# Optimization experiments

Hardware: AMD Instinct MI355X
Metric: run time of the kernel (lower is better)

Reference implementation:

```python
import jax, jax.numpy as jnp
import numpy as np

EPS = 1e-6


def _rmsnorm(x, w, eps=EPS):
    # x: (..., d); normalize over last dim
    ms = jnp.mean(jnp.square(x), axis=-1, keepdims=True)
    return x * jax.lax.rsqrt(ms + eps) * w


def setup_inputs() -> dict:
    key = jax.random.key(0)
    ks = jax.random.split(key, 5)
    B, S, D = 2, 2048, 2048
    n_heads, n_kv = 16, 4
    d_head = D // n_heads  # 128
    sd = 1.0 / np.sqrt(D)
    return {
        "x": jax.random.normal(ks[0], (B, S, D), dtype=jnp.float32),
        "wq": jax.random.normal(ks[1], (D, n_heads * d_head), dtype=jnp.float32) * sd,
        "wk": jax.random.normal(ks[2], (D, n_kv * d_head), dtype=jnp.float32) * sd,
        "wv": jax.random.normal(ks[3], (D, n_kv * d_head), dtype=jnp.float32) * sd,
        "wo": jax.random.normal(ks[4], (D, D), dtype=jnp.float32) * sd,
        "q_norm_w": jnp.ones((d_head,), dtype=jnp.float32),
        "k_norm_w": jnp.ones((d_head,), dtype=jnp.float32),
    }


def reference(x, wq, wk, wv, wo, q_norm_w, k_norm_w):
    B, S, D = x.shape
    n_heads, n_kv = 16, 4
    groups = n_heads // n_kv
    d_head = D // n_heads

    # QKV projections (bias=False)
    q = (x @ wq).reshape(B, S, n_kv, groups, d_head)  # q heads grouped by kv head
    k = (x @ wk).reshape(B, S, n_kv, d_head)
    v = (x @ wv).reshape(B, S, n_kv, d_head)

    # qk RMSNorm over d_head
    q = _rmsnorm(q, q_norm_w)
    k = _rmsnorm(k, k_norm_w)

    # GQA attention without materializing expanded K/V:
    # scores: (B, n_kv, groups, S_q, S_k)
    scale = 1.0 / jnp.sqrt(jnp.asarray(d_head, dtype=x.dtype))
    scores = jnp.einsum('bskgd,btkd->bkgst', q, k) * scale
    causal = jnp.tril(jnp.ones((S, S), dtype=bool))
    scores = jnp.where(causal, scores, jnp.asarray(-jnp.inf, dtype=scores.dtype))
    attn = jax.nn.softmax(scores, axis=-1)
    out = jnp.einsum('bkgst,btkd->bskgd', attn, v)  # (B, S, n_kv, groups, d_head)
    out = out.reshape(B, S, D)
    return out @ wo
```

## Files before the change

kernel.cpp:

```cpp
#include <hip/hip_runtime.h>
#include <hip/hip_bf16.h>
#include <stdint.h>

typedef unsigned short u16;
typedef __attribute__((ext_vector_type(8))) short short8;
typedef __attribute__((ext_vector_type(4))) float f32x4;
typedef __attribute__((ext_vector_type(16))) float f32x16;

__device__ __forceinline__ u16 f2bf(float f){
  union { __hip_bfloat16 h; u16 u; } v; v.h = __float2bfloat16(f); return v.u;
}
__device__ __forceinline__ float bf2f(u16 h){
  union { uint32_t u; float f; } v; v.u = ((uint32_t)h) << 16;
  return v.f;
}
__device__ __forceinline__ f32x4 mfma16(short8 a, short8 b, f32x4 c){
  return __builtin_amdgcn_mfma_f32_16x16x32_bf16(a, b, c, 0, 0, 0);
}
__device__ __forceinline__ f32x16 mfma32(short8 a, short8 b, f32x16 c){
  return __builtin_amdgcn_mfma_f32_32x32x16_bf16(a, b, c, 0, 0, 0);
}
__device__ __forceinline__ void gl_lds16(const u16* g, u16* l){
  __builtin_amdgcn_global_load_lds((const __attribute__((address_space(1))) void*)g,
                                   (__attribute__((address_space(3))) void*)l, 16, 0, 0);
}
template<int N> __device__ __forceinline__ void waitvm(){
  if constexpr (N==0) asm volatile("s_waitcnt vmcnt(0)" ::: "memory");
  else if constexpr (N==2) asm volatile("s_waitcnt vmcnt(2)" ::: "memory");
  else if constexpr (N==4) asm volatile("s_waitcnt vmcnt(4)" ::: "memory");
  else if constexpr (N==8) asm volatile("s_waitcnt vmcnt(8)" ::: "memory");
  else static_assert(N==0 || N==2 || N==4 || N==8, "unsupported vmcnt");
}
__device__ __forceinline__ void phase_sep(){
  __builtin_amdgcn_sched_barrier(0);
  __builtin_amdgcn_s_barrier();
  __builtin_amdgcn_sched_barrier(0);
}
__device__ __forceinline__ uint32_t cvtpk(float lo, float hi){
  uint32_t r;
  asm("v_cvt_pk_bf16_f32 %0, %1, %2" : "=v"(r) : "v"(lo), "v"(hi));
  return r;
}

__global__ __launch_bounds__(256) void prep(const float* __restrict__ x,
    const float* __restrict__ wq, const float* __restrict__ wk,
    const float* __restrict__ wv, const float* __restrict__ wo,
    u16* __restrict__ xbf, u16* __restrict__ wqkvT, u16* __restrict__ woT)
{
  __shared__ float tile[32][33];
  int bid = blockIdx.x;
  const int tid = threadIdx.x;
  if (bid < 8192){
    const int i = bid*256 + tid;
    const float4 v = ((const float4*)x)[i];
    ushort4 pk;
    pk.x = f2bf(v.x); pk.y = f2bf(v.y); pk.z = f2bf(v.z); pk.w = f2bf(v.w);
    ((ushort4*)xbf)[i] = pk;
    return;
  }
  bid -= 8192;
  const float* src; u16* dst; int C, bx, by;
  if (bid < 4096){ src = wq; dst = wqkvT; C = 2048; bx = bid & 63; by = bid >> 6; }
  else if (bid < 8192){ bid -= 4096; src = wo; dst = woT; C = 2048; bx = bid & 63; by = bid >> 6; }
  else if (bid < 9216){ bid -= 8192; src = wk; dst = wqkvT + 2048*2048; C = 512; bx = bid & 15; by = bid >> 4; }
  else { bid -= 9216; src = wv; dst = wqkvT + 2560*2048; C = 512; bx = bid & 15; by = bid >> 4; }
  const int R = 2048;
  const int tx = tid & 31, ty = tid >> 5;
  const int c0 = bx << 5, r0 = by << 5;
  #pragma unroll
  for (int i=0;i<4;i++)
    tile[ty + (i<<3)][tx] = src[(size_t)(r0 + ty + (i<<3))*C + c0 + tx];
  __syncthreads();
  #pragma unroll
  for (int i=0;i<4;i++)
    dst[(size_t)(c0 + ty + (i<<3))*R + r0 + tx] = f2bf(tile[tx][ty + (i<<3)]);
}

__global__ __launch_bounds__(256) void norm_vt(u16* __restrict__ qkv,
    const float* __restrict__ kw, u16* __restrict__ vT)
{
  const int tid = threadIdx.x;
  int bid = blockIdx.x;
  if (bid < 4096){
    const int lane = tid & 63;
    const int rid = bid*4 + (tid >> 6);
    const int row = rid >> 2;
    const int slot = rid & 3;
    u16* p = qkv + (size_t)row*3072 + 2048 + slot*128 + (lane<<1);
    const u16 r0 = p[0], r1 = p[1];
    const float a = bf2f(r0), c = bf2f(r1);
    float ss = a*a + c*c;
    #pragma unroll
    for (int off=1; off<64; off<<=1) ss += __shfl_xor(ss, off);
    const float sc = rsqrtf(ss*(1.0f/128.0f) + 1e-6f);
    const float w0 = kw[lane<<1], w1 = kw[(lane<<1)+1];
    p[0] = f2bf(a*sc*w0);
    p[1] = f2bf(c*sc*w1);
    return;
  }
  bid -= 4096;
  __shared__ u16 tile[32][33];
  const int tx = tid & 31, ty = tid >> 5;
  const int s0 = (bid & 63) << 5;
  const int d0 = ((bid >> 6) & 3) << 5;
  const int bk = bid >> 8; const int b = bk >> 2, kv = bk & 3;
  const u16* src = qkv + (size_t)b*2048*3072 + 2560 + kv*128;
  #pragma unroll
  for (int i=0;i<4;i++)
    tile[ty + (i<<3)][tx] = src[(size_t)(s0 + ty + (i<<3))*3072 + d0 + tx];
  __syncthreads();
  u16* dst = vT + (size_t)((b<<2)+kv)*128*2048;
  #pragma unroll
  for (int i=0;i<4;i++)
    dst[(size_t)(d0 + ty + (i<<3))*2048 + s0 + tx] = tile[tx][ty + (i<<3)];
}

__global__ __launch_bounds__(512, 2) void gemm192(const u16* __restrict__ A,
    const u16* __restrict__ BT, u16* __restrict__ Cp,
    int M, int N, int K, int ldc)
{
  constexpr int ASZ  = 128*64;
  constexpr int BSZ  = 64*64;
  constexpr int DBUF = 2*ASZ + 3*BSZ;
  __shared__ u16 lds[2*DBUF];
  const int tid = threadIdx.x;
  const int w = tid >> 6, lane = tid & 63;
  const int l15 = lane & 15, lg = lane >> 4;
  const int wm = w >> 2, wn = w & 3;
  const int nbx = N / 192;
  const int nwg = gridDim.x;
  int bid = blockIdx.x;
  bid = (bid & 7) * (nwg >> 3) + (bid >> 3);
  const int m0 = (bid / nbx) << 8;
  const int n0 = (bid % nbx) * 192;

  const u16* gA0 = A  + (size_t)m0*K;
  const u16* gA1 = gA0 + (size_t)128*K;
  const u16* gB  = BT + (size_t)n0*K;

  auto slotA = [&](int d, int h)->u16*{ return lds + d*DBUF + h*ASZ; };
  auto slotB = [&](int d, int s)->u16*{ return lds + d*DBUF + 2*ASZ + s*BSZ; };

  auto stage128 = [&](const u16* gbase, int kt, u16* sbase){
    #pragma unroll
    for (int i=0;i<2;i++){
      const int p = (i<<9) + tid;
      const int row = p>>3, sg = (p&7) ^ (row&7);
      gl_lds16(gbase + (size_t)row*K + (kt<<6) + (sg<<3), sbase + (p<<3));
    }
  };
  auto stage64 = [&](const u16* gbase, int kt, u16* sbase){
    const int row = tid>>3, sg = (tid&7) ^ (row&7);
    gl_lds16(gbase + (size_t)row*K + (kt<<6) + (sg<<3), sbase + (tid<<3));
  };
  auto stA = [&](int kt, int d){ stage128(gA0, kt, slotA(d,0));
                                 stage128(gA1, kt, slotA(d,1)); };
  auto stB = [&](int kt, int d){ stage64(gB,               kt, slotB(d,0));
                                 stage64(gB + (size_t) 64*K, kt, slotB(d,1));
                                 stage64(gB + (size_t)128*K, kt, slotB(d,2)); };
  auto frag_at = [&](const u16* buf, int lrow, int kk)->short8{
    const int s = ((kk<<2)+lg) ^ (lrow&7);
    return *(const short8*)(buf + (((lrow<<3)+s)<<3));
  };

  short8 af[4][2], bfe[2][2], bfo[2];
  f32x4 acc[8][3];
  #pragma unroll
  for (int m=0;m<8;m++)
    #pragma unroll
    for (int n=0;n<3;n++) acc[m][n] = (f32x4){0.f,0.f,0.f,0.f};

  auto rd_a = [&](int d, int mq){
    #pragma unroll
    for (int m=0;m<4;m++)
      #pragma unroll
      for (int kk=0;kk<2;kk++)
        af[m][kk] = frag_at(slotA(d,wm), (mq<<6) + (m<<4) + l15, kk);
  };
  auto rd_be = [&](int d){
    #pragma unroll
    for (int n=0;n<2;n++){
      const int r = wn*48 + (n<<4) + l15;
      #pragma unroll
      for (int kk=0;kk<2;kk++)
        bfe[n][kk] = frag_at(slotB(d, r>>6), r&63, kk);
    }
  };
  auto rd_bo = [&](int d){
    const int r = wn*48 + 32 + l15;
    #pragma unroll
    for (int kk=0;kk<2;kk++)
      bfo[kk] = frag_at(slotB(d, r>>6), r&63, kk);
  };
  auto mf_e = [&](int mb){
    __builtin_amdgcn_s_setprio(1);
    #pragma unroll
    for (int m=0;m<4;m++)
      #pragma unroll
      for (int n=0;n<2;n++)
        #pragma unroll
        for (int kk=0;kk<2;kk++)
          acc[mb+m][n] = mfma16(af[m][kk], bfe[n][kk], acc[mb+m][n]);
    __builtin_amdgcn_s_setprio(0);
  };
  auto mf_o = [&](int mb){
    __builtin_amdgcn_s_setprio(1);
    #pragma unroll
    for (int m=0;m<4;m++)
      #pragma unroll
      for (int kk=0;kk<2;kk++)
        acc[mb+m][2] = mfma16(af[m][kk], bfo[kk], acc[mb+m][2]);
    __builtin_amdgcn_s_setprio(0);
  };

  stA(0,0); stB(0,0); stA(1,1);
  waitvm<4>();
  phase_sep();

  const int niter = K >> 7;
  for (int i=0; i<niter; ++i){
    const bool full = (i+1 < niter);
    const int t1 = 2*i+1;
    rd_a(0, 0); rd_be(0);
    stB(t1, 1);
    phase_sep();
    mf_e(0);
    phase_sep();
    rd_bo(0);
    phase_sep();
    mf_o(0);
    phase_sep();
    rd_a(0, 1);
    phase_sep();
    mf_o(4);
    phase_sep();
    rd_be(0);
    if (full) stA(t1+1, 0);
    phase_sep();
    mf_e(4);
    if (full) waitvm<4>(); else waitvm<0>();
    phase_sep();
    rd_a(1, 0); rd_be(1);
    if (full) stB(t1+1, 0);
    phase_sep();
    mf_e(0);
    phase_sep();
    rd_bo(1);
    phase_sep();
    mf_o(0);
    phase_sep();
    rd_a(1, 1);
    phase_sep();
    mf_o(4);
    phase_sep();
    rd_be(1);
    if (full) stA(t1+2, 1);
    phase_sep();
    mf_e(4);
    if (full) waitvm<4>();
    phase_sep();
  }

  #pragma unroll
  for (int m=0;m<8;m++){
    #pragma unroll
    for (int n=0;n<3;n++){
      const int col = n0 + wn*48 + (n<<4) + l15;
      #pragma unroll
      for (int r=0;r<4;r++){
        const int row = m0 + (wm<<7) + (m<<4) + (lg<<2) + r;
        Cp[(size_t)row*ldc + col] = f2bf(acc[m][n][r]);
      }
    }
  }
}

template<int BM, int CBF16>
__global__ __launch_bounds__(512, 2) void gemm8(const u16* __restrict__ A,
    const u16* __restrict__ BT, void* __restrict__ Cp,
    int M, int N, int K, int ldc)
{
  constexpr int MF   = BM/32;
  constexpr int MQ   = MF/2;
  constexpr int AH   = BM/2;
  constexpr int ASZ  = AH*64;
  constexpr int DBUF = 2*ASZ + 16384;
  constexpr int WV   = (BM==256) ? 4 : 2;
  __shared__ u16 lds[2*DBUF];
  const int tid = threadIdx.x;
  const int w = tid >> 6, lane = tid & 63;
  const int l15 = lane & 15, lg = lane >> 4;
  const int wm = w >> 2, wn = w & 3;
  const int nbx = N >> 8;
  const int nwg = gridDim.x;
  int bid = blockIdx.x;
  bid = (bid & 7) * (nwg >> 3) + (bid >> 3);
  const int m0 = (bid / nbx) * BM;
  const int n0 = (bid % nbx) << 8;

  const u16* gA0 = A  + (size_t)m0*K;
  const u16* gA1 = gA0 + (size_t)AH*K;
  const u16* gB0 = BT + (size_t)n0*K;
  const u16* gB1 = gB0 + (size_t)128*K;

  auto slotA = [&](int d, int h)->u16*{ return lds + d*DBUF + h*ASZ; };
  auto slotB = [&](int d, int h)->u16*{ return lds + d*DBUF + 2*ASZ + h*8192; };

  auto stage_half = [&](const u16* gbase, int kt, u16* sbase, int rows){
    const int iters = rows >> 6;
    for (int i=0;i<iters;i++){
      const int p = (i<<9) + tid;
      const int row = p>>3, sg = (p&7) ^ (row&7);
      gl_lds16(gbase + (size_t)row*K + (kt<<6) + (sg<<3), sbase + (p<<3));
    }
  };
  auto stA = [&](int kt, int d){ stage_half(gA0, kt, slotA(d,0), AH);
                                 stage_half(gA1, kt, slotA(d,1), AH); };
  auto stB = [&](int kt, int d){ stage_half(gB0, kt, slotB(d,0), 128);
                                 stage_half(gB1, kt, slotB(d,1), 128); };
  auto frag_at = [&](const u16* buf, int lrow, int kk)->short8{
    const int s = ((kk<<2)+lg) ^ (lrow&7);
    return *(const short8*)(buf + (((lrow<<3)+s)<<3));
  };

  short8 af[MQ][2], bfe[2][2], bfo[2][2];
  f32x4 acc[MF][4];
  #pragma unroll
  for (int m=0;m<MF;m++)
    #pragma unroll
    for (int n=0;n<4;n++) acc[m][n] = (f32x4){0.f,0.f,0.f,0.f};

  const int bh = wn>>1;
  const int brow0 = ((wn&1)<<6) + l15;

  auto rd_a = [&](const u16* buf, int mq){
    #pragma unroll
    for (int m=0;m<MQ;m++)
      #pragma unroll
      for (int kk=0;kk<2;kk++)
        af[m][kk] = frag_at(buf, mq*(BM>>2) + (m<<4) + l15, kk);
  };
  auto rd_b = [&](const u16* buf, int nq, short8 (*dst)[2]){
    #pragma unroll
    for (int n=0;n<2;n++)
      #pragma unroll
      for (int kk=0;kk<2;kk++)
        dst[n][kk] = frag_at(buf, brow0 + (nq<<5) + (n<<4), kk);
  };
  auto do_mfma = [&](int mb, int nb, short8 (*bf)[2]){
    __builtin_amdgcn_s_setprio(1);
    #pragma unroll
    for (int m=0;m<MQ;m++)
      #pragma unroll
      for (int n=0;n<2;n++)
        #pragma unroll
        for (int kk=0;kk<2;kk++)
          acc[mb+m][nb+n] = mfma16(af[m][kk], bf[n][kk], acc[mb+m][nb+n]);
    __builtin_amdgcn_s_setprio(0);
  };

  stA(0,0); stB(0,0); stA(1,1);
  waitvm<WV>();
  phase_sep();

  const int niter = K >> 7;
  for (int i=0; i<niter; ++i){
    const bool full = (i+1 < niter);
    const int t1 = 2*i+1;
    rd_a(slotA(0,wm), 0); rd_b(slotB(0,bh), 0, bfe);
    stB(t1, 1);
    phase_sep();
    do_mfma(0, 0, bfe);
    phase_sep();
    rd_b(slotB(0,bh), 1, bfo);
    phase_sep();
    do_mfma(0, 2, bfo);
    phase_sep();
    rd_a(slotA(0,wm), 1);
    phase_sep();
    do_mfma(MQ, 2, bfo);
    phase_sep();
    rd_b(slotB(0,bh), 0, bfe);
    if (full) stA(t1+1, 0);
    phase_sep();
    do_mfma(MQ, 0, bfe);
    if (full) waitvm<WV>(); else waitvm<0>();
    phase_sep();
    rd_a(slotA(1,wm), 0); rd_b(slotB(1,bh), 0, bfe);
    if (full) stB(t1+1, 0);
    phase_sep();
    do_mfma(0, 0, bfe);
    phase_sep();
    rd_b(slotB(1,bh), 1, bfo);
    phase_sep();
    do_mfma(0, 2, bfo);
    phase_sep();
    rd_a(slotA(1,wm), 1);
    phase_sep();
    do_mfma(MQ, 2, bfo);
    phase_sep();
    rd_b(slotB(1,bh), 0, bfe);
    if (full) stA(t1+2, 1);
    phase_sep();
    do_mfma(MQ, 0, bfe);
    if (full) waitvm<WV>();
    phase_sep();
  }

  #pragma unroll
  for (int m=0;m<MF;m++){
    #pragma unroll
    for (int n=0;n<4;n++){
      const int col = n0 + (wn<<6) + (n<<4) + l15;
      #pragma unroll
      for (int r=0;r<4;r++){
        const int row = m0 + wm*AH + (m<<4) + (lg<<2) + r;
        if (CBF16) ((u16*)Cp)[(size_t)row*ldc + col] = f2bf(acc[m][n][r]);
        else       ((float*)Cp)[(size_t)row*ldc + col] = acc[m][n][r];
      }
    }
  }
}

__global__ __launch_bounds__(256, 2) void attn_kernel(const u16* __restrict__ qkv,
    const u16* __restrict__ vT, const float* __restrict__ qw,
    u16* __restrict__ aout)
{
  __shared__ u16 Klds[2][8192];
  __shared__ u16 Vlds[8192];
  const int tid = threadIdx.x;
  const int w = tid >> 6, lane = tid & 63;
  const int l31 = lane & 31, hi = lane >> 5;
  const int bx = blockIdx.x, h = blockIdx.y, b = blockIdx.z;
  const int qI = b ? bx : (15 - bx);
  const int kvh = h >> 2;
  const int qb = qI*128 + (w<<5);
  const int nt = 2*qI + 2;

  const u16* qkvb = qkv + (size_t)b*2048*3072;
  short8 qf[8];
  {
    const u16* qp = qkvb + (size_t)(qb + l31)*3072 + h*128 + hi*8;
    #pragma unroll
    for (int kk=0;kk<8;kk++) qf[kk] = *(const short8*)(qp + kk*16);
    float ss = 0.f;
    #pragma unroll
    for (int kk=0;kk<8;kk++)
      #pragma unroll
      for (int e=0;e<8;e++){
        const float v = bf2f((u16)qf[kk][e]);
        ss += v*v;
      }
    ss += __shfl_xor(ss, 32);
    const float sc = rsqrtf(ss*(1.0f/128.0f) + 1e-6f) * 0.1275187952317199f;
    #pragma unroll
    for (int kk=0;kk<8;kk++){
      #pragma unroll
      for (int e=0;e<8;e++){
        const float wv_ = qw[kk*16 + hi*8 + e];
        qf[kk][e] = (short)f2bf(bf2f((u16)qf[kk][e]) * sc * wv_);
      }
    }
  }
  f32x16 oacc[4];
  #pragma unroll
  for (int d=0;d<4;d++)
    #pragma unroll
    for (int r=0;r<16;r++) oacc[d][r] = 0.f;
  float m_run = -__builtin_inff(), lsum = 0.f;

  const u16* kb_ = qkvb + 2048 + kvh*128;
  const u16* vb_ = vT + (size_t)((b<<2)+kvh)*128*2048;

  auto stageK = [&](int t, int buf){
    #pragma unroll
    for (int i=0;i<4;i++){
      const int u = (i<<8) + tid;
      const int row = u>>4, d0 = (u&15) ^ (row&15);
      gl_lds16(kb_ + (size_t)((t<<6)+row)*3072 + (d0<<3), &Klds[buf][u<<3]);
    }
  };
  auto stageV = [&](int t){
    #pragma unroll
    for (int i=0;i<4;i++){
      const int u = (i<<8) + tid;
      const int rp = u>>4, z = (u&15) ^ (rp&15);
      const int d = (rp<<1) + (z>>3), k8 = z&7;
      gl_lds16(vb_ + (size_t)d*2048 + (t<<6) + (k8<<3), &Vlds[u<<3]);
    }
  };

  stageK(0, 0);
  int kbuf = 0;
  for (int t=0; t<nt; ++t){
    const bool pre = (t+1 < nt);
    stageV(t);
    if (pre) stageK(t+1, kbuf^1);
    if (pre) waitvm<8>(); else waitvm<4>();
    phase_sep();
    const int t0 = t<<6;
    f32x16 s0, s1;
    #pragma unroll
    for (int r=0;r<16;r++){ s0[r] = 0.f; s1[r] = 0.f; }
    __builtin_amdgcn_s_setprio(1);
    #pragma unroll
    for (int kk=0;kk<8;kk++){
      const int d0 = (kk<<1) + hi;
      const short8 k0 = *(const short8*)&Klds[kbuf][((l31<<4) + (d0 ^ (l31&15)))<<3];
      s0 = mfma32(k0, qf[kk], s0);
      const int r1 = 32 + l31;
      const short8 k1 = *(const short8*)&Klds[kbuf][((r1<<4) + (d0 ^ (r1&15)))<<3];
      s1 = mfma32(k1, qf[kk], s1);
    }
    __builtin_amdgcn_s_setprio(0);
    if (t0 + 63 > qb){
      const int qrel = qb + l31 - t0;
      #pragma unroll
      for (int r=0;r<16;r++){
        const int kloc = (r&3) + ((r>>2)<<3) + (hi<<2);
        if (kloc      > qrel) s0[r] = -__builtin_inff();
        if (kloc + 32 > qrel) s1[r] = -__builtin_inff();
      }
    }
    float t8[8];
    #pragma unroll
    for (int i=0;i<8;i++) t8[i] = fmaxf(fmaxf(s0[i], s0[i+8]), fmaxf(s1[i], s1[i+8]));
    #pragma unroll
    for (int i=0;i<4;i++) t8[i] = fmaxf(t8[i], t8[i+4]);
    float mx = fmaxf(fmaxf(t8[0],t8[1]), fmaxf(t8[2],t8[3]));
    mx = fmaxf(mx, __shfl_xor(mx, 32));
    const bool noskip = !__all(mx - m_run <= 8.0f);
    const float mnew = noskip ? fmaxf(m_run, mx) : m_run;
    float rs = 0.f;
    #pragma unroll
    for (int i=0;i<16;i++){
      s0[i] = __builtin_amdgcn_exp2f(s0[i] - mnew);
      s1[i] = __builtin_amdgcn_exp2f(s1[i] - mnew);
      rs += s0[i] + s1[i];
    }
    rs += __shfl_xor(rs, 32);
    if (noskip){
      const float corr = __builtin_amdgcn_exp2f(m_run - mnew);
      m_run = mnew;
      lsum = lsum*corr + rs;
      #pragma unroll
      for (int r=0;r<16;r++){
        const float cr = __shfl(corr, (r&3) + ((r>>2)<<3) + (hi<<2));
        #pragma unroll
        for (int db=0;db<4;db++) oacc[db][r] *= cr;
      }
    } else {
      lsum += rs;
    }
    uint32_t paw[4][4];
    #pragma unroll
    for (int kk=0;kk<4;kk++){
      const int base = (kk&1)<<3;
      float v0,v1,v2,v3,v4,v5,v6,v7;
      if (kk<2){ v0=s0[base+0]; v1=s0[base+1]; v2=s0[base+2]; v3=s0[base+3];
                 v4=s0[base+4]; v5=s0[base+5]; v6=s0[base+6]; v7=s0[base+7]; }
      else     { v0=s1[base+0]; v1=s1[base+1]; v2=s1[base+2]; v3=s1[base+3];
                 v4=s1[base+4]; v5=s1[base+5]; v6=s1[base+6]; v7=s1[base+7]; }
      uint32_t a0 = cvtpk(v0, v1), a1 = cvtpk(v2, v3);
      uint32_t b0 = cvtpk(v4, v5), b1 = cvtpk(v6, v7);
      asm volatile("v_permlane32_swap_b32 %0, %1" : "+v"(a0), "+v"(b0));
      asm volatile("v_permlane32_swap_b32 %0, %1" : "+v"(a1), "+v"(b1));
      paw[kk][0] = a0; paw[kk][1] = a1; paw[kk][2] = b0; paw[kk][3] = b1;
    }
    if (pre) waitvm<4>(); else waitvm<0>();
    phase_sep();
    __builtin_amdgcn_s_setprio(1);
    #pragma unroll
    for (int kk=0;kk<4;kk++){
      union { uint32_t w[4]; short8 v; } pu;
      pu.w[0]=paw[kk][0]; pu.w[1]=paw[kk][1]; pu.w[2]=paw[kk][2]; pu.w[3]=paw[kk][3];
      const short8 pa = pu.v;
      #pragma unroll
      for (int db=0;db<4;db++){
        const int d = (db<<5) + l31, rp = d>>1;
        const int sl = (((d&1)<<3) | ((kk<<1)+hi)) ^ (rp&15);
        const short8 vv = *(const short8*)&Vlds[((rp<<4)+sl)<<3];
        oacc[db] = mfma32(pa, vv, oacc[db]);
      }
    }
    __builtin_amdgcn_s_setprio(0);
    phase_sep();
    kbuf ^= 1;
  }

  const float inv = 1.0f / lsum;
  #pragma unroll
  for (int r=0;r<16;r++){
    const int qr = (r&3) + ((r>>2)<<3) + (hi<<2);
    const float ivr = __shfl(inv, qr);
    u16* op = aout + (size_t)(b*2048 + qb + qr)*2048 + h*128 + l31;
    #pragma unroll
    for (int db=0;db<4;db++)
      op[db<<5] = f2bf(oacc[db][r] * ivr);
  }
}

extern "C" void kernel_launch(void* const* d_in, const int* in_sizes, int n_in,
                              void* d_out, int out_size, void* d_ws, size_t ws_size,
                              hipStream_t stream) {
  const float* x  = (const float*)d_in[0];
  const float* wq = (const float*)d_in[1];
  const float* wk = (const float*)d_in[2];
  const float* wv = (const float*)d_in[3];
  const float* wo = (const float*)d_in[4];
  const float* qw = (const float*)d_in[5];
  const float* kw = (const float*)d_in[6];
  char* ws = (char*)d_ws;
  u16* xbf   = (u16*)(ws);
  u16* wqkvT = (u16*)(ws + 16777216);
  u16* woT   = (u16*)(ws + 29360128);
  u16* qkv   = (u16*)(ws + 37748736);
  u16* vT    = (u16*)(ws + 62914560);
  float* out = (float*)d_out;

  prep<<<18432, 256, 0, stream>>>(x, wq, wk, wv, wo, xbf, wqkvT, woT);
  gemm192<<<256, 512, 0, stream>>>(xbf, wqkvT, qkv, 4096, 3072, 2048, 3072);
  norm_vt<<<6144, 256, 0, stream>>>(qkv, kw, vT);
  attn_kernel<<<dim3(16,16,2), 256, 0, stream>>>(qkv, vT, qw, xbf);
  gemm8<128,0><<<256, 512, 0, stream>>>(xbf, woT, out, 4096, 2048, 2048, 2048);
}
```

Measured before the change: 174.1 us.

## Split long causal attention query blocks into two KV halves with combine kernel

Query blocks 8-15, which have the most causal KV tiles, are split into two work items that each cover half of the KV range. A lookup table orders all 768 work items longest first. The split items write unnormalised fp32 partial outputs plus running max and sum into scratch, reusing the output buffer and a free workspace region, and a new combine kernel merges them with log-sum-exp weights. This targets load imbalance and the long tail in causal attention, at the cost of an extra launch and the partial-result memory traffic.

```diff
diff --git a/kernel.cpp b/kernel.cpp
--- a/kernel.cpp
+++ b/kernel.cpp
@@ -6,6 +6,10 @@
 typedef __attribute__((ext_vector_type(8))) short short8;
 typedef __attribute__((ext_vector_type(4))) float f32x4;
 typedef __attribute__((ext_vector_type(16))) float f32x16;
+
+__constant__ unsigned char TJ[24] = {
+  39, 15, 31, 14, 30, 38, 13, 29, 12, 28, 37, 11,
+  27, 10, 26, 36,  9, 25,  8, 24, 35, 34, 33, 32 };
 
 __device__ __forceinline__ u16 f2bf(float f){
   union { __hip_bfloat16 h; u16 u; } v; v.h = __float2bfloat16(f); return v.u;
@@ -424,18 +428,23 @@
 
 __global__ __launch_bounds__(256, 2) void attn_kernel(const u16* __restrict__ qkv,
     const u16* __restrict__ vT, const float* __restrict__ qw,
-    u16* __restrict__ aout)
+    u16* __restrict__ aout, float* __restrict__ partial, float2* __restrict__ mlbuf)
 {
   __shared__ u16 Klds[2][8192];
   __shared__ u16 Vlds[8192];
   const int tid = threadIdx.x;
   const int w = tid >> 6, lane = tid & 63;
   const int l31 = lane & 31, hi = lane >> 5;
-  const int bx = blockIdx.x, h = blockIdx.y, b = blockIdx.z;
-  const int qI = b ? bx : (15 - bx);
-  const int kvh = h >> 2;
+  const int bid = blockIdx.x;
+  const int j = bid >> 5;
+  const int grp = bid & 31;
+  const int b = grp >> 4, kvh = (grp >> 2) & 3, hh = grp & 3;
+  const int h = (kvh<<2) + hh;
+  const unsigned v_ = TJ[j];
+  const int qI = v_ & 15, s = v_ >> 4;
+  const int tb = (s == 1) ? (qI + 1) : 0;
+  const int te = (s == 0) ? (qI + 1) : (2*qI + 2);
   const int qb = qI*128 + (w<<5);
-  const int nt = 2*qI + 2;
 
   const u16* qkvb = qkv + (size_t)b*2048*3072;
   short8 qf[8];
@@ -490,10 +499,10 @@
     }
   };
 
-  stageK(0, 0);
+  stageK(tb, 0);
   int kbuf = 0;
-  for (int t=0; t<nt; ++t){
-    const bool pre = (t+1 < nt);
+  for (int t=tb; t<te; ++t){
+    const bool pre = (t+1 < te);
     stageV(t);
     if (pre) stageK(t+1, kbuf^1);
     if (pre) waitvm<8>(); else waitvm<4>();
@@ -588,15 +597,58 @@
     kbuf ^= 1;
   }
 
-  const float inv = 1.0f / lsum;
-  #pragma unroll
-  for (int r=0;r<16;r++){
-    const int qr = (r&3) + ((r>>2)<<3) + (hi<<2);
-    const float ivr = __shfl(inv, qr);
-    u16* op = aout + (size_t)(b*2048 + qb + qr)*2048 + h*128 + l31;
-    #pragma unroll
-    for (int db=0;db<4;db++)
-      op[db<<5] = f2bf(oacc[db][r] * ivr);
+  if (s == 2){
+    const float inv = 1.0f / lsum;
+    #pragma unroll
+    for (int r=0;r<16;r++){
+      const int qr = (r&3) + ((r>>2)<<3) + (hi<<2);
+      const float ivr = __shfl(inv, qr);
+      u16* op = aout + (size_t)(b*2048 + qI*128 + (w<<5) + qr)*2048 + h*128 + l31;
+      #pragma unroll
+      for (int db=0;db<4;db++)
+        op[db<<5] = f2bf(oacc[db][r] * ivr);
+    }
+  } else {
+    const int tau = (((b<<4) + h)<<3) + (qI - 8);
+    float* pO = partial + (size_t)((tau<<1)+s)*16384;
+    #pragma unroll
+    for (int r=0;r<16;r++){
+      const int qr = (r&3) + ((r>>2)<<3) + (hi<<2);
+      float* pr = pO + ((w<<5)+qr)*128 + l31;
+      #pragma unroll
+      for (int db=0;db<4;db++) pr[db<<5] = oacc[db][r];
+    }
+    if (hi == 0)
+      mlbuf[((tau<<1)+s)*128 + (w<<5) + l31] = make_float2(m_run, lsum);
+  }
+}
+
+__global__ __launch_bounds__(256) void attn_combine(const float* __restrict__ partial,
+    const float2* __restrict__ mlbuf, u16* __restrict__ aout)
+{
+  const int tau = blockIdx.x;
+  const int b = tau >> 7, h = (tau >> 3) & 15, qI = (tau & 7) + 8;
+  const int row = threadIdx.x >> 1;
+  const int c0 = (threadIdx.x & 1) << 6;
+  const float2 ml0 = mlbuf[(tau<<1)*128 + row];
+  const float2 ml1 = mlbuf[((tau<<1)+1)*128 + row];
+  const float M = fmaxf(ml0.x, ml1.x);
+  float w0 = __builtin_amdgcn_exp2f(ml0.x - M);
+  float w1 = __builtin_amdgcn_exp2f(ml1.x - M);
+  const float inv = 1.0f / (w0*ml0.y + w1*ml1.y);
+  w0 *= inv; w1 *= inv;
+  const float4* P0 = (const float4*)(partial + (size_t)(tau<<1)*16384 + row*128 + c0);
+  const float4* P1 = (const float4*)(partial + (size_t)((tau<<1)+1)*16384 + row*128 + c0);
+  ushort4* op = (ushort4*)(aout + (size_t)(b*2048 + qI*128 + row)*2048 + h*128 + c0);
+  #pragma unroll
+  for (int i=0;i<16;i++){
+    const float4 a = P0[i], c = P1[i];
+    ushort4 o;
+    o.x = f2bf(w0*a.x + w1*c.x);
+    o.y = f2bf(w0*a.y + w1*c.y);
+    o.z = f2bf(w0*a.z + w1*c.z);
+    o.w = f2bf(w0*a.w + w1*c.w);
+    op[i] = o;
   }
 }
 
@@ -616,11 +668,13 @@
   u16* woT   = (u16*)(ws + 29360128);
   u16* qkv   = (u16*)(ws + 37748736);
   u16* vT    = (u16*)(ws + 62914560);
+  float2* ml = (float2*)(ws + 16777216);
   float* out = (float*)d_out;
 
   prep<<<18432, 256, 0, stream>>>(x, wq, wk, wv, wo, xbf, wqkvT, woT);
   gemm192<<<256, 512, 0, stream>>>(xbf, wqkvT, qkv, 4096, 3072, 2048, 3072);
   norm_vt<<<6144, 256, 0, stream>>>(qkv, kw, vT);
-  attn_kernel<<<dim3(16,16,2), 256, 0, stream>>>(qkv, vT, qw, xbf);
+  attn_kernel<<<768, 256, 0, stream>>>(qkv, vT, qw, xbf, out, ml);
+  attn_combine<<<256, 256, 0, stream>>>(out, ml, xbf);
   gemm8<128,0><<<256, 512, 0, stream>>>(xbf, woT, out, 4096, 2048, 2048, 2048);
 }
```

New measurement: 188.1 us. 8.1% more time.
